# Kernel optimization log

Hardware: AMD Instinct MI355X
Metric: run time of the kernel (lower is better)

Reference implementation:

```python
import jax, jax.numpy as jnp
import numpy as np


def _gat_layer(h, mask, w, a_src, a_dst):
    # h: [B,C,N,Fin], w: [C,H,Fin,Fout], a_*: [C,H,Fout,1], mask: [B,N,N] (True where no edge)
    h_prime = jnp.einsum('bcni,chio->bchno', h, w)          # [B,C,H,N,Fout]
    t = jnp.tanh(h_prime)
    s = jnp.einsum('bchno,cho->bchn', t, a_src[..., 0])      # src scores
    d = jnp.einsum('bchno,cho->bchn', t, a_dst[..., 0])      # dst scores
    attn = s[..., :, None] + d[..., None, :]                 # [B,C,H,N,N]
    attn = jnp.where(attn >= 0, attn, 0.2 * attn)            # leaky_relu(0.2)
    attn = jnp.where(mask[:, None, None, :, :], jnp.float32(-1e12), attn)
    attn = jax.nn.softmax(attn, axis=-1)
    return jnp.einsum('bchnm,bchmo->bchno', attn, h_prime)   # [B,C,H,N,Fout]


def setup_inputs() -> dict:
    key = jax.random.key(0)
    ks = jax.random.split(key, 8)
    B, C, N, F0, H, F = 2, 2, 1024, 64, 8, 64

    def xavier(k, shape):
        fan_in, fan_out = shape[-2], shape[-1]
        lim = (6.0 / (fan_in + fan_out)) ** 0.5
        return jax.random.uniform(k, shape, jnp.float32, -lim, lim)

    x = jax.random.normal(ks[0], (B, C, N, F0), dtype=jnp.float32)
    adj = jax.random.randint(ks[1], (B, N, N), 0, 2, dtype=jnp.int32)
    w1 = xavier(ks[2], (C, H, F0, F))
    a_src1 = xavier(ks[3], (C, H, F, 1))
    a_dst1 = xavier(ks[4], (C, H, F, 1))
    w2 = xavier(ks[5], (C, H, H * F, F))
    a_src2 = xavier(ks[6], (C, H, F, 1))
    a_dst2 = xavier(ks[7], (C, H, F, 1))
    return {"x": x, "adj": adj, "w1": w1, "a_src1": a_src1, "a_dst1": a_dst1,
            "w2": w2, "a_src2": a_src2, "a_dst2": a_dst2}


def reference(x, adj, w1, a_src1, a_dst1, w2, a_src2, a_dst2):
    B, C, N, _ = x.shape
    adj_f = adj.astype(jnp.float32) + jnp.eye(N, dtype=jnp.float32)[None]  # add self-loops
    mask = adj_f == 0                                        # [B,N,N]
    out1 = _gat_layer(x, mask, w1, a_src1, a_dst1)           # [B,C,H,N,F]
    # permute heads next to features, flatten, elu (dropout is identity in eval)
    x1 = jax.nn.elu(jnp.transpose(out1, (0, 1, 3, 2, 4)).reshape(B, C, N, -1))
    out2 = _gat_layer(x1, mask, w2, a_src2, a_dst2)          # [B,C,H,N,F]
    return out2.mean(axis=2)                                 # mean over heads -> [B,C,N,F]
```

## Files before the change

kernel.cpp:

```cpp
#include <hip/hip_runtime.h>
#include <hip/hip_bf16.h>

#define BB 2
#define CC 2
#define NN 1024
#define F0V 64
#define HH 8
#define FFV 64
#define BCHN (BB*CC*HH)
#define SVN  (BB*CC*HH*NN)

typedef _Float16 f16x8 __attribute__((ext_vector_type(8)));
typedef _Float16 f16x4 __attribute__((ext_vector_type(4)));
typedef __fp16 h16x2 __attribute__((ext_vector_type(2)));
typedef float f32x4 __attribute__((ext_vector_type(4)));

__global__ __launch_bounds__(256) void prep_kernel(
    const float* __restrict__ x, const int* __restrict__ adj,
    const float* __restrict__ w1, const float* __restrict__ w2,
    _Float16* __restrict__ xh, _Float16* __restrict__ w1T, _Float16* __restrict__ w2T,
    unsigned long long* __restrict__ bmg)
{
  __shared__ __align__(16) _Float16 tile[64*72];
  const int bx = blockIdx.x;
  const int t = threadIdx.x;
  if (bx < 256) {
    const int i = bx*256 + t;
    const float4 v = ((const float4*)x)[i];
    f16x4 o; o[0]=(_Float16)v.x; o[1]=(_Float16)v.y; o[2]=(_Float16)v.z; o[3]=(_Float16)v.w;
    ((f16x4*)xh)[i] = o;
  } else if (bx < 400) {
    int ch, k0, K; const float* w; _Float16* wT;
    if (bx < 272) { ch = bx - 256; k0 = 0; K = 64; w = w1; wT = w1T; }
    else { const int u = bx - 272; ch = u >> 3; k0 = (u & 7)*64; K = 512; w = w2; wT = w2T; }
    const float* src = w + ((size_t)ch*K + k0)*64;
    #pragma unroll
    for (int j = 0; j < 4; ++j) {
      const int u = t + j*256;
      const int k = u >> 4, seg = u & 15;
      const float4 v = ((const float4*)src)[(size_t)k*16 + seg];
      tile[(seg*4+0)*72 + k] = (_Float16)v.x;
      tile[(seg*4+1)*72 + k] = (_Float16)v.y;
      tile[(seg*4+2)*72 + k] = (_Float16)v.z;
      tile[(seg*4+3)*72 + k] = (_Float16)v.w;
    }
    __syncthreads();
    _Float16* dst = wT + (size_t)ch*64*K + k0;
    #pragma unroll
    for (int j = 0; j < 2; ++j) {
      const int u = t + j*256;
      const int f = u >> 3, seg = u & 7;
      const f16x8 o = *(const f16x8*)&tile[f*72 + seg*8];
      *(f16x8*)(dst + (size_t)f*K + seg*8) = o;
    }
  } else {
    const int wg = (bx - 400)*4 + (t >> 6);
    const int lane = t & 63;
    for (int idx = wg; idx < BB*NN*16; idx += 1024) {
      const int b = idx >> 14;
      const int n = (idx >> 4) & (NN - 1);
      const int word = idx & 15;
      const int m = word*64 + lane;
      const int pred = (adj[((size_t)b*NN + n)*NN + m] != 0) || (m == n);
      unsigned long long bits = __ballot(pred);
      if (lane == 0) bmg[idx] = bits;
    }
  }
}

template<int K>
__global__ __launch_bounds__(256) void proj_mfma(
    const _Float16* __restrict__ A,
    const _Float16* __restrict__ wT,
    const float* __restrict__ asrc, const float* __restrict__ adst,
    _Float16* __restrict__ HpT, float* __restrict__ s_out, float* __restrict__ d_out)
{
  __shared__ float sp[4][32], sd[4][32];
  const int bch = blockIdx.y;
  const int h = bch % HH; const int bc = bch / HH; const int c = bc % CC;
  const int row0 = blockIdx.x*32;
  const int t = threadIdx.x;
  const int w = t >> 6, lane = t & 63;
  const int colr = lane & 15, quad = lane >> 4;

  const _Float16* Arow0 = A + ((size_t)bc*NN + row0 + colr)*K;
  const _Float16* Arow1 = Arow0 + (size_t)16*K;
  const _Float16* Brow  = wT + ((size_t)(c*HH + h)*64 + w*16 + colr)*K;

  f32x4 acc0 = {0.f,0.f,0.f,0.f}, acc1 = {0.f,0.f,0.f,0.f};
  #pragma unroll 4
  for (int kb = 0; kb < K; kb += 32) {
    const f16x8 a0 = *(const f16x8*)(Arow0 + kb + quad*8);
    const f16x8 a1 = *(const f16x8*)(Arow1 + kb + quad*8);
    const f16x8 bf = *(const f16x8*)(Brow  + kb + quad*8);
    acc0 = __builtin_amdgcn_mfma_f32_16x16x32_f16(a0, bf, acc0, 0, 0, 0);
    acc1 = __builtin_amdgcn_mfma_f32_16x16x32_f16(a1, bf, acc1, 0, 0, 0);
  }

  const float af = asrc[(c*HH + h)*64 + w*16 + colr];
  const float bf_ = adst[(c*HH + h)*64 + w*16 + colr];
  _Float16* HT = HpT + ((size_t)bch*64 + w*16 + colr)*NN + row0;

  #pragma unroll
  for (int mt = 0; mt < 2; ++mt) {
    const f32x4 a = mt ? acc1 : acc0;
    f16x4 hv;
    #pragma unroll
    for (int i = 0; i < 4; ++i) {
      const float v = a[i];
      hv[i] = (_Float16)v;
      const float ex = __expf(2.f*v);
      const float th = 1.f - 2.f/(ex + 1.f);
      float ps = th * af, pd = th * bf_;
      #pragma unroll
      for (int off = 1; off < 16; off <<= 1) {
        ps += __shfl_xor(ps, off);
        pd += __shfl_xor(pd, off);
      }
      if (colr == 0) {
        sp[w][mt*16 + quad*4 + i] = ps;
        sd[w][mt*16 + quad*4 + i] = pd;
      }
    }
    *(f16x4*)(HT + mt*16 + quad*4) = hv;
  }
  __syncthreads();
  if (t < 32) {
    const float sv = sp[0][t] + sp[1][t] + sp[2][t] + sp[3][t];
    const float dv = sd[0][t] + sd[1][t] + sd[2][t] + sd[3][t];
    s_out[bch*NN + row0 + t] = sv;
    d_out[bch*NN + row0 + t] = dv;
  }
}

template<int LAYER>
__global__ __launch_bounds__(256, 4) void attn_mfma(
    const _Float16* __restrict__ HpT, const float* __restrict__ s_arr,
    const float* __restrict__ d_arr, const unsigned long long* __restrict__ bmg,
    _Float16* __restrict__ outp)
{
  __shared__ float partials[4][32*68];
  __shared__ float dsP[4][32];
  const int bch = blockIdx.x;
  const int b = bch / (CC*HH);
  const int row0 = blockIdx.y*32;
  const int t = threadIdx.x;
  const int w = t >> 6, lane = t & 63;
  const int colr = lane & 15, quad = lane >> 4;

  const float* dg = d_arr + (size_t)bch*NN;
  const float4* dg4 = (const float4*)dg;
  float mxl = -1e30f;
  #pragma unroll
  for (int j = 0; j < 4; ++j) {
    const float4 v = dg4[lane + 64*j];
    mxl = fmaxf(fmaxf(v.x, v.y), fmaxf(fmaxf(v.z, v.w), mxl));
  }
  #pragma unroll
  for (int off = 1; off < 64; off <<= 1) mxl = fmaxf(mxl, __shfl_xor(mxl, off));
  const float maxd = mxl;

  const int r0 = row0 + colr, r1 = r0 + 16;
  const float s0 = s_arr[(size_t)bch*NN + r0];
  const float s1 = s_arr[(size_t)bch*NN + r1];
  const float so0 = s0 + maxd, so1 = s1 + maxd;
  const float offs0 = fmaxf(so0, 0.2f*so0);
  const float offs1 = fmaxf(so1, 0.2f*so1);
  const float sA0 = s0 - offs0, sB0 = 0.2f*s0 - offs0;
  const float sA1 = s1 - offs1, sB1 = 0.2f*s1 - offs1;

  unsigned long long m0[4], m1[4];
  {
    const unsigned long long* bm0 = bmg + ((size_t)b*NN + r0)*16 + w*4;
    const unsigned long long* bm1 = bmg + ((size_t)b*NN + r1)*16 + w*4;
    #pragma unroll
    for (int j = 0; j < 4; ++j) { m0[j] = bm0[j]; m1[j] = bm1[j]; }
  }

  const _Float16* Bg = HpT + (size_t)bch*64*NN;
  const int kbase = w*256;
  const _Float16* Bp = Bg + kbase + quad*8;

  f32x4 acc[2][4], accs[2];
  #pragma unroll
  for (int rt = 0; rt < 2; ++rt) {
    accs[rt] = (f32x4){0.f,0.f,0.f,0.f};
    #pragma unroll
    for (int ft = 0; ft < 4; ++ft) acc[rt][ft] = (f32x4){0.f,0.f,0.f,0.f};
  }
  f16x8 ones;
  #pragma unroll
  for (int i = 0; i < 8; ++i) ones[i] = (_Float16)1.f;

  f16x8 Bc[4];
  #pragma unroll
  for (int ft = 0; ft < 4; ++ft) Bc[ft] = *(const f16x8*)(Bp + (size_t)(ft*16 + colr)*NN);
  float4 dc0 = *(const float4*)(dg + kbase + quad*8);
  float4 dc1 = *(const float4*)(dg + kbase + quad*8 + 4);

  #pragma unroll
  for (int ks = 0; ks < 8; ++ks) {
    f16x8 Bn[4]; float4 dn0, dn1;
    if (ks < 7) {
      #pragma unroll
      for (int ft = 0; ft < 4; ++ft)
        Bn[ft] = *(const f16x8*)(Bp + (size_t)(ft*16 + colr)*NN + (ks+1)*32);
      dn0 = *(const float4*)(dg + kbase + (ks+1)*32 + quad*8);
      dn1 = *(const float4*)(dg + kbase + (ks+1)*32 + quad*8 + 4);
    }
    const unsigned mb0 = (unsigned)((m0[ks >> 1] >> ((ks & 1)*32 + quad*8)) & 0xFFull);
    const unsigned mb1 = (unsigned)((m1[ks >> 1] >> ((ks & 1)*32 + quad*8)) & 0xFFull);
    const float dd[8] = {dc0.x, dc0.y, dc0.z, dc0.w, dc1.x, dc1.y, dc1.z, dc1.w};
    union { f16x8 v; h16x2 h[4]; } A0, A1;
    #pragma unroll
    for (int jp = 0; jp < 4; ++jp) {
      float p0[2], p1[2];
      #pragma unroll
      for (int jj = 0; jj < 2; ++jj) {
        const int j = jp*2 + jj;
        const float dj = dd[j];
        const float l0 = fmaxf(sA0 + dj, fmaf(0.2f, dj, sB0));
        const float l1 = fmaxf(sA1 + dj, fmaf(0.2f, dj, sB1));
        p0[jj] = ((mb0 >> j) & 1u) ? __expf(l0) : 0.f;
        p1[jj] = ((mb1 >> j) & 1u) ? __expf(l1) : 0.f;
      }
      A0.h[jp] = __builtin_amdgcn_cvt_pkrtz(p0[0], p0[1]);
      A1.h[jp] = __builtin_amdgcn_cvt_pkrtz(p1[0], p1[1]);
    }
    #pragma unroll
    for (int ft = 0; ft < 4; ++ft) {
      acc[0][ft] = __builtin_amdgcn_mfma_f32_16x16x32_f16(A0.v, Bc[ft], acc[0][ft], 0, 0, 0);
      acc[1][ft] = __builtin_amdgcn_mfma_f32_16x16x32_f16(A1.v, Bc[ft], acc[1][ft], 0, 0, 0);
    }
    accs[0] = __builtin_amdgcn_mfma_f32_16x16x32_f16(A0.v, ones, accs[0], 0, 0, 0);
    accs[1] = __builtin_amdgcn_mfma_f32_16x16x32_f16(A1.v, ones, accs[1], 0, 0, 0);
    if (ks < 7) {
      #pragma unroll
      for (int ft = 0; ft < 4; ++ft) Bc[ft] = Bn[ft];
      dc0 = dn0; dc1 = dn1;
    }
  }

  if (colr == 0) {
    #pragma unroll
    for (int i = 0; i < 4; ++i) {
      dsP[w][quad*4 + i] = accs[0][i];
      dsP[w][16 + quad*4 + i] = accs[1][i];
    }
  }
  float* pw = partials[w];
  #pragma unroll
  for (int rt = 0; rt < 2; ++rt)
    #pragma unroll
    for (int ft = 0; ft < 4; ++ft)
      #pragma unroll
      for (int i = 0; i < 4; ++i)
        pw[(rt*16 + quad*4 + i)*68 + ft*16 + colr] = acc[rt][ft][i];
  __syncthreads();

  const int r = t >> 3, f0 = (t & 7)*8;
  const float dsum = dsP[0][r] + dsP[1][r] + dsP[2][r] + dsP[3][r];
  const float inv = 1.f / dsum;
  float4 c0 = {0.f,0.f,0.f,0.f}, c1 = {0.f,0.f,0.f,0.f};
  #pragma unroll
  for (int w4 = 0; w4 < 4; ++w4) {
    const float* base = &partials[w4][r*68 + f0];
    const float4 a0 = *(const float4*)base;
    const float4 a1 = *(const float4*)(base + 4);
    c0.x += a0.x; c0.y += a0.y; c0.z += a0.z; c0.w += a0.w;
    c1.x += a1.x; c1.y += a1.y; c1.z += a1.z; c1.w += a1.w;
  }
  const float cv[8] = {c0.x,c0.y,c0.z,c0.w, c1.x,c1.y,c1.z,c1.w};
  f16x8 o;
  #pragma unroll
  for (int i = 0; i < 8; ++i) {
    float v = cv[i] * inv;
    if (LAYER == 1) v = v > 0.f ? v : expm1f(v);
    o[i] = (_Float16)v;
  }
  const int bc = bch / HH, h = bch % HH;
  if (LAYER == 1)
    *(f16x8*)(outp + ((size_t)bc*NN + row0 + r)*512 + h*64 + f0) = o;
  else
    *(f16x8*)(outp + ((size_t)bch*NN + row0 + r)*64 + f0) = o;
}

__global__ __launch_bounds__(256) void reduce_heads(
    const _Float16* __restrict__ out2, float* __restrict__ out)
{
  const int o = blockIdx.x*256 + threadIdx.x;
  const int f = o & 63;
  const int n = (o >> 6) & (NN - 1);
  const int bc = o >> 16;
  float acc = 0.f;
  #pragma unroll
  for (int h = 0; h < HH; ++h)
    acc += (float)out2[(((size_t)bc*HH + h)*NN + n)*FFV + f];
  out[o] = acc * 0.125f;
}

extern "C" void kernel_launch(void* const* d_in, const int* in_sizes, int n_in,
                              void* d_out, int out_size, void* d_ws, size_t ws_size,
                              hipStream_t stream)
{
  const float* x   = (const float*)d_in[0];
  const int*   adj = (const int*)d_in[1];
  const float* w1  = (const float*)d_in[2];
  const float* as1 = (const float*)d_in[3];
  const float* ad1 = (const float*)d_in[4];
  const float* w2  = (const float*)d_in[5];
  const float* as2 = (const float*)d_in[6];
  const float* ad2 = (const float*)d_in[7];

  char* w8 = (char*)d_ws;
  _Float16* HpT = (_Float16*)(w8);
  _Float16* XB  = (_Float16*)(w8 + (4u<<20));
  _Float16* xh  = (_Float16*)(w8 + (8u<<20));
  _Float16* w1T = (_Float16*)(w8 + (8u<<20) + (512u<<10));
  _Float16* w2T = (_Float16*)(w8 + (8u<<20) + (768u<<10));
  float* s_v = (float*)(w8 + (10u<<20));
  float* d_v = (float*)(w8 + (10u<<20) + SVN*4);
  unsigned long long* bmg = (unsigned long long*)(w8 + (10u<<20) + SVN*8);

  prep_kernel<<<656, 256, 0, stream>>>(x, adj, w1, w2, xh, w1T, w2T, bmg);
  proj_mfma<64><<<dim3(NN/32, BCHN), 256, 0, stream>>>(xh, w1T, as1, ad1, HpT, s_v, d_v);
  attn_mfma<1><<<dim3(BCHN, NN/32), 256, 0, stream>>>(HpT, s_v, d_v, bmg, XB);
  proj_mfma<512><<<dim3(NN/32, BCHN), 256, 0, stream>>>(XB, w2T, as2, ad2, HpT, s_v, d_v);
  attn_mfma<2><<<dim3(BCHN, NN/32), 256, 0, stream>>>(HpT, s_v, d_v, bmg, XB);
  reduce_heads<<<dim3((unsigned)(out_size/256)), 256, 0, stream>>>(XB, (float*)d_out);
}
```

Measured before the change: 164.9 us.

## Fuse x fp16 conversion into proj1 and head-mean into layer-2 attention

Drops the separate x→fp16 conversion pass; proj1 now reads fp32 x and converts in registers with packed round-to-zero conversion. Also removes the reduce_heads launch: in layer-2 attention, the last of the 8 head blocks per row tile (found with an atomic counter and threadfences) sums the heads and writes the final output. This removes one kernel launch and one global round trip. In exchange it adds atomics and fence ordering, and counters that prep resets on every call.

After: 293.8 us. 1.78x slower.

```diff
diff --git a/kernel.cpp b/kernel.cpp
--- a/kernel.cpp
+++ b/kernel.cpp
@@ -4,7 +4,6 @@
 #define BB 2
 #define CC 2
 #define NN 1024
-#define F0V 64
 #define HH 8
 #define FFV 64
 #define BCHN (BB*CC*HH)
@@ -16,23 +15,17 @@
 typedef float f32x4 __attribute__((ext_vector_type(4)));
 
 __global__ __launch_bounds__(256) void prep_kernel(
-    const float* __restrict__ x, const int* __restrict__ adj,
-    const float* __restrict__ w1, const float* __restrict__ w2,
-    _Float16* __restrict__ xh, _Float16* __restrict__ w1T, _Float16* __restrict__ w2T,
-    unsigned long long* __restrict__ bmg)
+    const int* __restrict__ adj, const float* __restrict__ w1, const float* __restrict__ w2,
+    _Float16* __restrict__ w1T, _Float16* __restrict__ w2T,
+    unsigned long long* __restrict__ bmg, int* __restrict__ cnt)
 {
   __shared__ __align__(16) _Float16 tile[64*72];
   const int bx = blockIdx.x;
   const int t = threadIdx.x;
-  if (bx < 256) {
-    const int i = bx*256 + t;
-    const float4 v = ((const float4*)x)[i];
-    f16x4 o; o[0]=(_Float16)v.x; o[1]=(_Float16)v.y; o[2]=(_Float16)v.z; o[3]=(_Float16)v.w;
-    ((f16x4*)xh)[i] = o;
-  } else if (bx < 400) {
+  if (bx < 144) {
     int ch, k0, K; const float* w; _Float16* wT;
-    if (bx < 272) { ch = bx - 256; k0 = 0; K = 64; w = w1; wT = w1T; }
-    else { const int u = bx - 272; ch = u >> 3; k0 = (u & 7)*64; K = 512; w = w2; wT = w2T; }
+    if (bx < 16) { ch = bx; k0 = 0; K = 64; w = w1; wT = w1T; }
+    else { const int u = bx - 16; ch = u >> 3; k0 = (u & 7)*64; K = 512; w = w2; wT = w2T; }
     const float* src = w + ((size_t)ch*K + k0)*64;
     #pragma unroll
     for (int j = 0; j < 4; ++j) {
@@ -53,8 +46,8 @@
       const f16x8 o = *(const f16x8*)&tile[f*72 + seg*8];
       *(f16x8*)(dst + (size_t)f*K + seg*8) = o;
     }
-  } else {
-    const int wg = (bx - 400)*4 + (t >> 6);
+  } else if (bx < 400) {
+    const int wg = (bx - 144)*4 + (t >> 6);
     const int lane = t & 63;
     for (int idx = wg; idx < BB*NN*16; idx += 1024) {
       const int b = idx >> 14;
@@ -65,12 +58,13 @@
       unsigned long long bits = __ballot(pred);
       if (lane == 0) bmg[idx] = bits;
     }
+  } else {
+    if (t < 128) cnt[t] = 0;
   }
 }
 
-template<int K>
-__global__ __launch_bounds__(256) void proj_mfma(
-    const _Float16* __restrict__ A,
+__global__ __launch_bounds__(256) void proj1_mfma(
+    const float* __restrict__ x,
     const _Float16* __restrict__ wT,
     const float* __restrict__ asrc, const float* __restrict__ adst,
     _Float16* __restrict__ HpT, float* __restrict__ s_out, float* __restrict__ d_out)
@@ -83,6 +77,82 @@
   const int w = t >> 6, lane = t & 63;
   const int colr = lane & 15, quad = lane >> 4;
 
+  const float* Ar0 = x + ((size_t)bc*NN + row0 + colr)*64;
+  const float* Ar1 = Ar0 + (size_t)16*64;
+  const _Float16* Brow = wT + ((size_t)(c*HH + h)*64 + w*16 + colr)*64;
+
+  f32x4 acc0 = {0.f,0.f,0.f,0.f}, acc1 = {0.f,0.f,0.f,0.f};
+  #pragma unroll
+  for (int kb = 0; kb < 64; kb += 32) {
+    const float4 u0 = *(const float4*)(Ar0 + kb + quad*8);
+    const float4 u1 = *(const float4*)(Ar0 + kb + quad*8 + 4);
+    const float4 v0 = *(const float4*)(Ar1 + kb + quad*8);
+    const float4 v1 = *(const float4*)(Ar1 + kb + quad*8 + 4);
+    union { f16x8 v; h16x2 h[4]; } a0, a1;
+    a0.h[0] = __builtin_amdgcn_cvt_pkrtz(u0.x, u0.y);
+    a0.h[1] = __builtin_amdgcn_cvt_pkrtz(u0.z, u0.w);
+    a0.h[2] = __builtin_amdgcn_cvt_pkrtz(u1.x, u1.y);
+    a0.h[3] = __builtin_amdgcn_cvt_pkrtz(u1.z, u1.w);
+    a1.h[0] = __builtin_amdgcn_cvt_pkrtz(v0.x, v0.y);
+    a1.h[1] = __builtin_amdgcn_cvt_pkrtz(v0.z, v0.w);
+    a1.h[2] = __builtin_amdgcn_cvt_pkrtz(v1.x, v1.y);
+    a1.h[3] = __builtin_amdgcn_cvt_pkrtz(v1.z, v1.w);
+    const f16x8 bf = *(const f16x8*)(Brow + kb + quad*8);
+    acc0 = __builtin_amdgcn_mfma_f32_16x16x32_f16(a0.v, bf, acc0, 0, 0, 0);
+    acc1 = __builtin_amdgcn_mfma_f32_16x16x32_f16(a1.v, bf, acc1, 0, 0, 0);
+  }
+
+  const float af = asrc[(c*HH + h)*64 + w*16 + colr];
+  const float bf_ = adst[(c*HH + h)*64 + w*16 + colr];
+  _Float16* HT = HpT + ((size_t)bch*64 + w*16 + colr)*NN + row0;
+
+  #pragma unroll
+  for (int mt = 0; mt < 2; ++mt) {
+    const f32x4 a = mt ? acc1 : acc0;
+    f16x4 hv;
+    #pragma unroll
+    for (int i = 0; i < 4; ++i) {
+      const float v = a[i];
+      hv[i] = (_Float16)v;
+      const float ex = __expf(2.f*v);
+      const float th = 1.f - 2.f/(ex + 1.f);
+      float ps = th * af, pd = th * bf_;
+      #pragma unroll
+      for (int off = 1; off < 16; off <<= 1) {
+        ps += __shfl_xor(ps, off);
+        pd += __shfl_xor(pd, off);
+      }
+      if (colr == 0) {
+        sp[w][mt*16 + quad*4 + i] = ps;
+        sd[w][mt*16 + quad*4 + i] = pd;
+      }
+    }
+    *(f16x4*)(HT + mt*16 + quad*4) = hv;
+  }
+  __syncthreads();
+  if (t < 32) {
+    const float sv = sp[0][t] + sp[1][t] + sp[2][t] + sp[3][t];
+    const float dv = sd[0][t] + sd[1][t] + sd[2][t] + sd[3][t];
+    s_out[bch*NN + row0 + t] = sv;
+    d_out[bch*NN + row0 + t] = dv;
+  }
+}
+
+__global__ __launch_bounds__(256) void proj2_mfma(
+    const _Float16* __restrict__ A,
+    const _Float16* __restrict__ wT,
+    const float* __restrict__ asrc, const float* __restrict__ adst,
+    _Float16* __restrict__ HpT, float* __restrict__ s_out, float* __restrict__ d_out)
+{
+  const int K = 512;
+  __shared__ float sp[4][32], sd[4][32];
+  const int bch = blockIdx.y;
+  const int h = bch % HH; const int bc = bch / HH; const int c = bc % CC;
+  const int row0 = blockIdx.x*32;
+  const int t = threadIdx.x;
+  const int w = t >> 6, lane = t & 63;
+  const int colr = lane & 15, quad = lane >> 4;
+
   const _Float16* Arow0 = A + ((size_t)bc*NN + row0 + colr)*K;
   const _Float16* Arow1 = Arow0 + (size_t)16*K;
   const _Float16* Brow  = wT + ((size_t)(c*HH + h)*64 + w*16 + colr)*K;
@@ -137,10 +207,11 @@
 __global__ __launch_bounds__(256, 4) void attn_mfma(
     const _Float16* __restrict__ HpT, const float* __restrict__ s_arr,
     const float* __restrict__ d_arr, const unsigned long long* __restrict__ bmg,
-    _Float16* __restrict__ outp)
+    _Float16* __restrict__ outp, int* __restrict__ cnt, float* __restrict__ outF)
 {
   __shared__ float partials[4][32*68];
   __shared__ float dsP[4][32];
+  __shared__ int is_last;
   const int bch = blockIdx.x;
   const int b = bch / (CC*HH);
   const int row0 = blockIdx.y*32;
@@ -279,24 +350,34 @@
     o[i] = (_Float16)v;
   }
   const int bc = bch / HH, h = bch % HH;
-  if (LAYER == 1)
+  if (LAYER == 1) {
     *(f16x8*)(outp + ((size_t)bc*NN + row0 + r)*512 + h*64 + f0) = o;
-  else
+  } else {
     *(f16x8*)(outp + ((size_t)bch*NN + row0 + r)*64 + f0) = o;
-}
-
-__global__ __launch_bounds__(256) void reduce_heads(
-    const _Float16* __restrict__ out2, float* __restrict__ out)
-{
-  const int o = blockIdx.x*256 + threadIdx.x;
-  const int f = o & 63;
-  const int n = (o >> 6) & (NN - 1);
-  const int bc = o >> 16;
-  float acc = 0.f;
-  #pragma unroll
-  for (int h = 0; h < HH; ++h)
-    acc += (float)out2[(((size_t)bc*HH + h)*NN + n)*FFV + f];
-  out[o] = acc * 0.125f;
+    __threadfence();
+    if (t == 0) {
+      const int gid = bc*32 + (row0 >> 5);
+      const int old = atomicAdd(&cnt[gid], 1);
+      is_last = (old == 7);
+    }
+    __syncthreads();
+    if (is_last) {
+      __threadfence();
+      float accm[8] = {0.f,0.f,0.f,0.f,0.f,0.f,0.f,0.f};
+      #pragma unroll
+      for (int hh = 0; hh < HH; ++hh) {
+        const f16x8 v = *(const f16x8*)(outp + (((size_t)bc*HH + hh)*NN + row0 + r)*64 + f0);
+        #pragma unroll
+        for (int i = 0; i < 8; ++i) accm[i] += (float)v[i];
+      }
+      float4 o0, o1;
+      o0.x = accm[0]*0.125f; o0.y = accm[1]*0.125f; o0.z = accm[2]*0.125f; o0.w = accm[3]*0.125f;
+      o1.x = accm[4]*0.125f; o1.y = accm[5]*0.125f; o1.z = accm[6]*0.125f; o1.w = accm[7]*0.125f;
+      float* dst = outF + ((size_t)bc*NN + row0 + r)*64 + f0;
+      *(float4*)dst = o0;
+      *(float4*)(dst + 4) = o1;
+    }
+  }
 }
 
 extern "C" void kernel_launch(void* const* d_in, const int* in_sizes, int n_in,
@@ -315,17 +396,16 @@
   char* w8 = (char*)d_ws;
   _Float16* HpT = (_Float16*)(w8);
   _Float16* XB  = (_Float16*)(w8 + (4u<<20));
-  _Float16* xh  = (_Float16*)(w8 + (8u<<20));
-  _Float16* w1T = (_Float16*)(w8 + (8u<<20) + (512u<<10));
-  _Float16* w2T = (_Float16*)(w8 + (8u<<20) + (768u<<10));
+  _Float16* w1T = (_Float16*)(w8 + (8u<<20));
+  _Float16* w2T = (_Float16*)(w8 + (8u<<20) + (256u<<10));
   float* s_v = (float*)(w8 + (10u<<20));
   float* d_v = (float*)(w8 + (10u<<20) + SVN*4);
   unsigned long long* bmg = (unsigned long long*)(w8 + (10u<<20) + SVN*8);
-
-  prep_kernel<<<656, 256, 0, stream>>>(x, adj, w1, w2, xh, w1T, w2T, bmg);
-  proj_mfma<64><<<dim3(NN/32, BCHN), 256, 0, stream>>>(xh, w1T, as1, ad1, HpT, s_v, d_v);
-  attn_mfma<1><<<dim3(BCHN, NN/32), 256, 0, stream>>>(HpT, s_v, d_v, bmg, XB);
-  proj_mfma<512><<<dim3(NN/32, BCHN), 256, 0, stream>>>(XB, w2T, as2, ad2, HpT, s_v, d_v);
-  attn_mfma<2><<<dim3(BCHN, NN/32), 256, 0, stream>>>(HpT, s_v, d_v, bmg, XB);
-  reduce_heads<<<dim3((unsigned)(out_size/256)), 256, 0, stream>>>(XB, (float*)d_out);
+  int* cnt = (int*)(w8 + (10u<<20) + SVN*8 + (256u<<10));
+
+  prep_kernel<<<401, 256, 0, stream>>>(adj, w1, w2, w1T, w2T, bmg, cnt);
+  proj1_mfma<<<dim3(NN/32, BCHN), 256, 0, stream>>>(x, w1T, as1, ad1, HpT, s_v, d_v);
+  attn_mfma<1><<<dim3(BCHN, NN/32), 256, 0, stream>>>(HpT, s_v, d_v, bmg, XB, cnt, (float*)d_out);
+  proj2_mfma<<<dim3(NN/32, BCHN), 256, 0, stream>>>(XB, w2T, as2, ad2, HpT, s_v, d_v);
+  attn_mfma<2><<<dim3(BCHN, NN/32), 256, 0, stream>>>(HpT, s_v, d_v, bmg, XB, cnt, (float*)d_out);
 }
```
